# Kernel tuning notes

Measured on AMD Instinct MI355X. Metric: run time of the kernel, lower is better.

The kernel has to match this reference:

```python
import jax, jax.numpy as jnp
import numpy as np

V, E, H, L = 32000, 512, 512, 2   # vocab, emb_dim, hidden_dim, lstm layers
IN = 2 * H                        # input_size (= enc_output feature dim)
B, S_ENC, T_DEC = 32, 128, 64


def setup_inputs() -> dict:
    key = jax.random.key(0)
    ks = jax.random.split(key, 20)
    sc = 0.05
    inp = {
        "tokens": jax.random.randint(ks[0], (B, T_DEC), 0, V),
        "enc_output": jax.random.normal(ks[1], (B, S_ENC, IN), jnp.float32),
        "enc_h": jax.random.normal(ks[2], (L, B, H), jnp.float32),
        "enc_c": jax.random.normal(ks[3], (L, B, H), jnp.float32),
        "emb": jax.random.normal(ks[4], (V, E), jnp.float32) * sc,
        # attention MLP: attn1 in = H*L + IN, out = 4H; attn2: 4H -> 1
        "attn1_w": jax.random.normal(ks[5], (4 * H, H * L + IN), jnp.float32) * sc,
        "attn1_b": jnp.zeros((4 * H,), jnp.float32),
        "attn2_w": jax.random.normal(ks[6], (1, 4 * H), jnp.float32) * sc,
        "attn2_b": jnp.zeros((1,), jnp.float32),
        # LSTM layer 0: input E + IN; layer 1: input H. PyTorch gate order i,f,g,o
        "w_ih0": jax.random.normal(ks[7], (4 * H, E + IN), jnp.float32) * sc,
        "w_hh0": jax.random.normal(ks[8], (4 * H, H), jnp.float32) * sc,
        "b_ih0": jnp.zeros((4 * H,), jnp.float32),
        "b_hh0": jnp.zeros((4 * H,), jnp.float32),
        "w_ih1": jax.random.normal(ks[9], (4 * H, H), jnp.float32) * sc,
        "w_hh1": jax.random.normal(ks[10], (4 * H, H), jnp.float32) * sc,
        "b_ih1": jnp.zeros((4 * H,), jnp.float32),
        "b_hh1": jnp.zeros((4 * H,), jnp.float32),
        "out_w": jax.random.normal(ks[11], (V, H), jnp.float32) * sc,
        "out_b": jnp.zeros((V,), jnp.float32),
    }
    return inp


def _lstm_cell(x, h, c, w_ih, w_hh, b_ih, b_hh):
    g = x @ w_ih.T + h @ w_hh.T + (b_ih + b_hh)
    i, f, gg, o = jnp.split(g, 4, axis=-1)
    c_new = jax.nn.sigmoid(f) * c + jax.nn.sigmoid(i) * jnp.tanh(gg)
    h_new = jax.nn.sigmoid(o) * jnp.tanh(c_new)
    return h_new, c_new


def reference(tokens, enc_output, enc_h, enc_c, emb,
              attn1_w, attn1_b, attn2_w, attn2_b,
              w_ih0, w_hh0, b_ih0, b_hh0,
              w_ih1, w_hh1, b_ih1, b_hh1,
              out_w, out_b):
    b, s_enc = enc_output.shape[0], enc_output.shape[1]

    def context(h):  # h: [L, B, H] -> context: [B, 2H]
        hflat = jnp.transpose(h, (1, 0, 2)).reshape(b, -1)          # [B, L*H]
        hexp = jnp.broadcast_to(hflat[:, None, :], (b, s_enc, hflat.shape[-1]))
        ai = jnp.concatenate([enc_output, hexp], axis=-1)           # [B, S, 2H+L*H]
        hid = ai @ attn1_w.T + attn1_b                               # [B, S, 4H]
        logits = hid @ attn2_w.T + attn2_b                           # [B, S, 1]
        w = jax.nn.softmax(logits, axis=1)
        return jnp.sum(enc_output * w, axis=1)                       # [B, 2H]

    def step(carry, emb_t):  # emb_t: [B, E]
        h, c = carry
        ctx = context(h)
        x = jnp.concatenate([emb_t, ctx], axis=-1)                   # [B, E+2H]
        h0, c0 = _lstm_cell(x, h[0], c[0], w_ih0, w_hh0, b_ih0, b_hh0)
        h1, c1 = _lstm_cell(h0, h[1], c[1], w_ih1, w_hh1, b_ih1, b_hh1)
        return (jnp.stack([h0, h1]), jnp.stack([c0, c1])), h1

    emb_seq = jnp.transpose(emb[tokens], (1, 0, 2))                  # [T, B, E]
    _, outs = jax.lax.scan(step, (enc_h, enc_c), emb_seq)            # [T, B, H]
    dec = jnp.transpose(outs, (1, 0, 2))                             # [B, T, H]
    return dec @ out_w.T + out_b                                     # [B, T, V]
```

## Files before the change

kernel.cpp:

```cpp
#include <hip/hip_runtime.h>
#include <hip/hip_bf16.h>

typedef __attribute__((ext_vector_type(4))) float f4v;
typedef __attribute__((ext_vector_type(4))) short s4v;
typedef __attribute__((ext_vector_type(8))) short s8v;

#define DEVINL __device__ __forceinline__
#define NBLK 128
#define PADK 536
#define WROWS (16 * PADK)
#define HSLOT 16384

DEVINL short f2bf(float f) {
  unsigned u = __float_as_uint(f);
  u += 0x7FFFu + ((u >> 16) & 1u);
  return (short)(u >> 16);
}
DEVINL float bf2f(short s) {
  return __uint_as_float(((unsigned)(unsigned short)s) << 16);
}
DEVINL float sigm(float x) { return 1.f / (1.f + expf(-x)); }

DEVINL void cstore64(short* p, unsigned long long d) {
  asm volatile("global_store_dwordx2 %0, %1, off sc0 sc1"
               :: "v"(p), "v"(d) : "memory");
}

__global__ __launch_bounds__(256) void k_init2(const float* __restrict__ enc_h,
                                               short* __restrict__ hbuf,
                                               unsigned* __restrict__ arr) {
  int i = blockIdx.x * 256 + threadIdx.x;
  hbuf[i] = f2bf(enc_h[i]);
  hbuf[(long)65 * HSLOT + i] = f2bf(enc_h[16384 + i]);
  if (i < NBLK * 32 + 32) arr[i] = 0u;
}

__global__ __launch_bounds__(256) void k_weff(const float* __restrict__ attn1_w,
                                              const float* __restrict__ attn2_w,
                                              float* __restrict__ w_enc) {
  __shared__ float part[8][32];
  int t = threadIdx.x;
  int jl = t & 31, kp = t >> 5;
  int j = blockIdx.x * 32 + jl;
  float acc = 0.f;
  for (int k = kp * 256; k < kp * 256 + 256; ++k)
    acc += attn2_w[k] * attn1_w[(long)k * 2048 + j];
  part[kp][jl] = acc;
  __syncthreads();
  if (t < 32) {
    float s = 0.f;
    for (int p = 0; p < 8; ++p) s += part[p][t];
    w_enc[blockIdx.x * 32 + t] = s;
  }
}

__global__ __launch_bounds__(256) void k_attn_lg(const float* __restrict__ enc,
                                                 const float* __restrict__ w_enc,
                                                 float* __restrict__ logits) {
  __shared__ float red[16][17];
  int b = blockIdx.x >> 3, sp = blockIdx.x & 7;
  int t = threadIdx.x, row = t >> 4, kc = t & 15;
  int s = sp * 16 + row;
  const float* e = enc + ((long)b * 128 + s) * 1024 + kc * 64;
  const float* wv = w_enc + kc * 64;
  float acc = 0.f;
  for (int k = 0; k < 64; k += 4) {
    f4v ev = *(const f4v*)(e + k);
    f4v w4 = *(const f4v*)(wv + k);
    acc += ev[0] * w4[0] + ev[1] * w4[1] + ev[2] * w4[2] + ev[3] * w4[3];
  }
  red[row][kc] = acc;
  __syncthreads();
  if (kc == 0) {
    float sm = 0.f;
#pragma unroll
    for (int i = 0; i < 16; ++i) sm += red[row][i];
    logits[b * 128 + s] = sm;
  }
}

__global__ __launch_bounds__(256) void k_attn_cx(const float* __restrict__ enc,
                                                 const float* __restrict__ logits,
                                                 float* __restrict__ ctx) {
  __shared__ float wls[128];
  __shared__ float red[256];
  int b = blockIdx.x >> 2, ch = blockIdx.x & 3;
  int t = threadIdx.x;
  float lv = (t < 128) ? logits[b * 128 + t] : -3.4e38f;
  red[t] = lv;
  __syncthreads();
  for (int off = 128; off >= 1; off >>= 1) {
    if (t < off) red[t] = fmaxf(red[t], red[t + off]);
    __syncthreads();
  }
  float mx = red[0];
  __syncthreads();
  float ex = 0.f;
  if (t < 128) { ex = expf(lv - mx); wls[t] = ex; }
  red[t] = ex;
  __syncthreads();
  for (int off = 128; off >= 1; off >>= 1) {
    if (t < off) red[t] += red[t + off];
    __syncthreads();
  }
  float inv = 1.f / red[0];
  int dim = ch * 256 + t;
  const float* eb = enc + (long)b * 131072 + dim;
  float a = 0.f;
#pragma unroll 4
  for (int ss = 0; ss < 128; ++ss) a += wls[ss] * eb[ss * 1024];
  ctx[b * 1024 + dim] = a * inv;
}

__global__ __launch_bounds__(256) void k_ctxpre(const float* __restrict__ w_ih0,
                                                const float* __restrict__ b_ih0,
                                                const float* __restrict__ b_hh0,
                                                const float* __restrict__ ctx,
                                                float* __restrict__ ctxpre) {
  int t = threadIdx.x;
  int j = blockIdx.x * 8 + (t >> 5);
  int b = t & 31;
  float acc = b_ih0[j] + b_hh0[j];
  const float* w = w_ih0 + (long)j * 1536 + 512;
  const float* c = ctx + b * 1024;
  for (int k = 0; k < 1024; k += 4) {
    f4v wv = *(const f4v*)(w + k);
    f4v cv = *(const f4v*)(c + k);
    acc += wv[0] * cv[0] + wv[1] * cv[1] + wv[2] * cv[2] + wv[3] * cv[3];
  }
  ctxpre[b * 2048 + j] = acc;
}

__global__ __launch_bounds__(256) void k_cvt(const float* __restrict__ src,
                                             short* __restrict__ dst) {
  long i = ((long)blockIdx.x * 256 + threadIdx.x) * 8;
  f4v a = *(const f4v*)(src + i);
  f4v b = *(const f4v*)(src + i + 4);
  s8v o;
  o[0] = f2bf(a[0]); o[1] = f2bf(a[1]); o[2] = f2bf(a[2]); o[3] = f2bf(a[3]);
  o[4] = f2bf(b[0]); o[5] = f2bf(b[1]); o[6] = f2bf(b[2]); o[7] = f2bf(b[3]);
  *(s8v*)(dst + i) = o;
}

template <int MODE>
__global__ __launch_bounds__(256) void gemm_bf16(
    const float* __restrict__ A, const float* __restrict__ B,
    const int* __restrict__ a_rows, const float* __restrict__ bias,
    float* __restrict__ C, int K, int lda, int ldb, int ldc) {
  __shared__ short As[128 * 72];
  __shared__ short Bs[128 * 72];
  int n0 = blockIdx.x * 128, m0 = blockIdx.y * 128;
  int t = threadIdx.x;
  int lane = t & 63, w = t >> 6;
  int wm = w & 1, wn = w >> 1;
  f4v acc[4][4];
#pragma unroll
  for (int mi = 0; mi < 4; ++mi)
#pragma unroll
    for (int ni = 0; ni < 4; ++ni) acc[mi][ni] = (f4v){0.f, 0.f, 0.f, 0.f};

  int sr = t >> 1;
  int sh = (t & 1) * 32;
  long arow = a_rows ? (long)a_rows[m0 + sr] : (long)(m0 + sr);
  const float* ap = A + arow * lda + sh;
  const float* bp = B + (long)(n0 + sr) * ldb + sh;
  short* as = &As[sr * 72 + sh];
  short* bs = &Bs[sr * 72 + sh];

  for (int k0 = 0; k0 < K; k0 += 64) {
#pragma unroll
    for (int i = 0; i < 8; ++i) {
      f4v va = *(const f4v*)(ap + k0 + i * 4);
      f4v vb = *(const f4v*)(bp + k0 + i * 4);
      s4v sa, sb;
      sa[0] = f2bf(va[0]); sa[1] = f2bf(va[1]); sa[2] = f2bf(va[2]); sa[3] = f2bf(va[3]);
      sb[0] = f2bf(vb[0]); sb[1] = f2bf(vb[1]); sb[2] = f2bf(vb[2]); sb[3] = f2bf(vb[3]);
      *(s4v*)(as + i * 4) = sa;
      *(s4v*)(bs + i * 4) = sb;
    }
    __syncthreads();
#pragma unroll
    for (int ks = 0; ks < 2; ++ks) {
      s8v af[4], bf[4];
#pragma unroll
      for (int mi = 0; mi < 4; ++mi)
        af[mi] = *(const s8v*)&As[(wm * 64 + mi * 16 + (lane & 15)) * 72 + ks * 32 + (lane >> 4) * 8];
#pragma unroll
      for (int ni = 0; ni < 4; ++ni)
        bf[ni] = *(const s8v*)&Bs[(wn * 64 + ni * 16 + (lane & 15)) * 72 + ks * 32 + (lane >> 4) * 8];
#pragma unroll
      for (int mi = 0; mi < 4; ++mi)
#pragma unroll
        for (int ni = 0; ni < 4; ++ni)
          acc[mi][ni] = __builtin_amdgcn_mfma_f32_16x16x32_bf16(af[mi], bf[ni], acc[mi][ni], 0, 0, 0);
    }
    __syncthreads();
  }
  int fq = lane >> 4, fr = lane & 15;
#pragma unroll
  for (int mi = 0; mi < 4; ++mi)
#pragma unroll
    for (int ni = 0; ni < 4; ++ni) {
      int col = n0 + wn * 64 + ni * 16 + fr;
      long rowb = m0 + wm * 64 + mi * 16 + fq * 4;
      if (MODE == 2) {
        int bz = (col & 511) >> 2;
        int c = ((col >> 9) << 2) + (col & 3);
#pragma unroll
        for (int r = 0; r < 4; ++r) {
          long m = rowb + r;
          C[(long)bz * 32768 + (m & 63) * 512 + (m >> 6) * 16 + c] = acc[mi][ni][r];
        }
      } else {
        float bv = bias ? bias[col] : 0.f;
#pragma unroll
        for (int r = 0; r < 4; ++r) C[(rowb + r) * (long)ldc + col] = acc[mi][ni][r] + bv;
      }
    }
}

template <bool BCVT>
__global__ __launch_bounds__(256) void gemm_out(
    const short* __restrict__ A, const short* __restrict__ Bbf,
    const float* __restrict__ Bf, const float* __restrict__ bias,
    float* __restrict__ C) {
  __shared__ short As[128 * 72];
  __shared__ short Bs[128 * 72];
  int m0 = blockIdx.x * 128, n0 = blockIdx.y * 128;
  int t = threadIdx.x;
  int lane = t & 63, w = t >> 6;
  int wm = w & 1, wn = w >> 1;
  f4v acc[4][4];
#pragma unroll
  for (int mi = 0; mi < 4; ++mi)
#pragma unroll
    for (int ni = 0; ni < 4; ++ni) acc[mi][ni] = (f4v){0.f, 0.f, 0.f, 0.f};

  int sr = t >> 1;
  int sh = (t & 1) * 32;
  const short* ap = A + (long)(m0 + sr) * 512 + sh;
  const short* bpb = Bbf + (long)(n0 + sr) * 512 + sh;
  const float* bpf = Bf + (long)(n0 + sr) * 512 + sh;
  short* as = &As[sr * 72 + sh];
  short* bs = &Bs[sr * 72 + sh];

  for (int k0 = 0; k0 < 512; k0 += 64) {
#pragma unroll
    for (int i = 0; i < 4; ++i)
      *(s8v*)(as + i * 8) = *(const s8v*)(ap + k0 + i * 8);
    if (BCVT) {
#pragma unroll
      for (int i = 0; i < 8; ++i) {
        f4v vb = *(const f4v*)(bpf + k0 + i * 4);
        s4v sb;
        sb[0] = f2bf(vb[0]); sb[1] = f2bf(vb[1]); sb[2] = f2bf(vb[2]); sb[3] = f2bf(vb[3]);
        *(s4v*)(bs + i * 4) = sb;
      }
    } else {
#pragma unroll
      for (int i = 0; i < 4; ++i)
        *(s8v*)(bs + i * 8) = *(const s8v*)(bpb + k0 + i * 8);
    }
    __syncthreads();
#pragma unroll
    for (int ks = 0; ks < 2; ++ks) {
      s8v af[4], bf[4];
#pragma unroll
      for (int mi = 0; mi < 4; ++mi)
        af[mi] = *(const s8v*)&As[(wm * 64 + mi * 16 + (lane & 15)) * 72 + ks * 32 + (lane >> 4) * 8];
#pragma unroll
      for (int ni = 0; ni < 4; ++ni)
        bf[ni] = *(const s8v*)&Bs[(wn * 64 + ni * 16 + (lane & 15)) * 72 + ks * 32 + (lane >> 4) * 8];
#pragma unroll
      for (int mi = 0; mi < 4; ++mi)
#pragma unroll
        for (int ni = 0; ni < 4; ++ni)
          acc[mi][ni] = __builtin_amdgcn_mfma_f32_16x16x32_bf16(af[mi], bf[ni], acc[mi][ni], 0, 0, 0);
    }
    __syncthreads();
  }
  int fq = lane >> 4, fr = lane & 15;
#pragma unroll
  for (int mi = 0; mi < 4; ++mi)
#pragma unroll
    for (int ni = 0; ni < 4; ++ni) {
      int col = n0 + wn * 64 + ni * 16 + fr;
      float bv = bias[col];
      long rowb = m0 + wm * 64 + mi * 16 + fq * 4;
#pragma unroll
      for (int r = 0; r < 4; ++r)
        __builtin_nontemporal_store(acc[mi][ni][r] + bv, &C[(rowb + r) * 32000L + col]);
    }
}

__global__ __launch_bounds__(256, 1) void lstm_persist(
    const float* __restrict__ w_hh0, const float* __restrict__ w_ih1,
    const float* __restrict__ w_hh1,
    const float* __restrict__ b_ih1, const float* __restrict__ b_hh1,
    const float* __restrict__ enc_c,
    const float* __restrict__ embp2, const float* __restrict__ ctxpre,
    short* __restrict__ hbuf, short* __restrict__ h1seqbf,
    unsigned* __restrict__ arr) {
  __shared__ alignas(16) short wlds[6 * WROWS];
  __shared__ float ctxp_l[32][16];
  __shared__ float bias1_l[16];
  __shared__ float gbuf[2][32][17];

  const int tid = threadIdx.x;
  const bool is_l0 = (blockIdx.x < NBLK);
  const int bz = is_l0 ? blockIdx.x : blockIdx.x - NBLK;
  const int hb4 = bz * 4;
  const int lane = tid & 63, wid = tid >> 6;
  const int mt = wid & 1, kh = wid >> 1;
  const int fr = lane & 15, fq = lane >> 4;

  const int nmat = is_l0 ? 1 : 2;
  for (int base = tid * 4; base < nmat * 16 * 512; base += 1024) {
    int row = base >> 9, k = base & 511;
    int m = row >> 4, c = row & 15;
    int j = ((c >> 2) << 9) + hb4 + (c & 3);
    const float* wsrc = is_l0 ? w_hh0 : (m == 0 ? w_ih1 : w_hh1);
    f4v v = *(const f4v*)(wsrc + (long)j * 512 + k);
    short* hi = &wlds[(m * 2) * WROWS + c * PADK + k];
    short* lo = &wlds[(m * 2 + 1) * WROWS + c * PADK + k];
#pragma unroll
    for (int e = 0; e < 4; ++e) {
      short hh = f2bf(v[e]);
      hi[e] = hh;
      lo[e] = f2bf(v[e] - bf2f(hh));
    }
  }
  if (is_l0) {
    for (int i = tid; i < 512; i += 256) {
      int b = i >> 4, c = i & 15;
      ctxp_l[b][c] = ctxpre[b * 2048 + ((c >> 2) << 9) + hb4 + (c & 3)];
    }
  } else if (tid < 16) {
    int j = ((tid >> 2) << 9) + hb4 + (tid & 3);
    bias1_l[tid] = b_ih1[j] + b_hh1[j];
  }
  const int cq = (tid & 127) >> 2, cr = tid & 3;
  float cst = 0.f;
  if (tid < 128)
    cst = enc_c[(is_l0 ? 0 : 16384) + cq * 512 + hb4 + cr];
  __syncthreads();
  asm volatile("s_waitcnt vmcnt(0)" ::: "memory");
  asm volatile("buffer_inv sc1" ::: "memory");
  __syncthreads();

  short* H0 = hbuf;
  short* H1 = hbuf + (long)65 * HSLOT;
  const int foff = (mt * 16 + fr) * 512 + kh * 256 + fq * 8;
  const int woff = fr * PADK + kh * 256 + fq * 8;

  if (is_l0) {
    for (int p = 0; p < 64; ++p) {
      float e4[4];
      if (tid < 128) {
        const float* ep = embp2 + (long)bz * 32768 + p * 512 + cq * 16 + cr;
#pragma unroll
        for (int g = 0; g < 4; ++g) e4[g] = ep[g * 4];
      }
      if (p) {
        if (tid < NBLK)
          while (__hip_atomic_load(&arr[tid << 5], __ATOMIC_RELAXED,
                                   __HIP_MEMORY_SCOPE_AGENT) < (unsigned)p)
            __builtin_amdgcn_s_sleep(1);
        __syncthreads();
      }
      const short* a0 = H0 + (long)p * HSLOT + foff;
      f4v l0h = {0.f, 0.f, 0.f, 0.f}, l0l = l0h;
      const short* b0h = &wlds[0 * WROWS + woff];
      const short* b0l = &wlds[1 * WROWS + woff];
#pragma unroll
      for (int ks = 0; ks < 8; ++ks) {
        s8v A0 = *(const s8v*)(a0 + ks * 32);
        s8v B0h = *(const s8v*)(b0h + ks * 32);
        s8v B0l = *(const s8v*)(b0l + ks * 32);
        l0h = __builtin_amdgcn_mfma_f32_16x16x32_bf16(A0, B0h, l0h, 0, 0, 0);
        l0l = __builtin_amdgcn_mfma_f32_16x16x32_bf16(A0, B0l, l0l, 0, 0, 0);
      }
      f4v s = l0h + l0l;
#pragma unroll
      for (int r = 0; r < 4; ++r) gbuf[kh][mt * 16 + fq * 4 + r][fr] = s[r];
      __syncthreads();
      if (tid < 128) {
        float g4[4];
#pragma unroll
        for (int g = 0; g < 4; ++g) {
          int c = g * 4 + cr;
          g4[g] = gbuf[0][cq][c] + gbuf[1][cq][c] + ctxp_l[cq][c] + e4[g];
        }
        float cn = sigm(g4[1]) * cst + sigm(g4[0]) * tanhf(g4[2]);
        float hn = sigm(g4[3]) * tanhf(cn);
        cst = cn;
        unsigned v16 = (unsigned)(unsigned short)f2bf(hn);
        unsigned p01 = v16 | ((unsigned)__shfl_down((int)v16, 1) << 16);
        unsigned long long wd = (unsigned long long)p01 |
            ((unsigned long long)(unsigned)__shfl_down((int)p01, 2) << 32);
        if ((tid & 3) == 0)
          cstore64(H0 + (long)(p + 1) * HSLOT + cq * 512 + hb4, wd);
      }
      asm volatile("s_waitcnt vmcnt(0)" ::: "memory");
      __syncthreads();
      if (tid == 0)
        __hip_atomic_store(&arr[(unsigned)bz << 5], (unsigned)(p + 1),
                           __ATOMIC_RELAXED, __HIP_MEMORY_SCOPE_AGENT);
    }
  } else {
    for (int p = 1; p <= 64; ++p) {
      if (tid < NBLK)
        while (__hip_atomic_load(&arr[tid << 5], __ATOMIC_RELAXED,
                                 __HIP_MEMORY_SCOPE_AGENT) < (unsigned)p)
          __builtin_amdgcn_s_sleep(2);
      __syncthreads();
      const short* a0 = H0 + (long)p * HSLOT + foff;
      f4v x1h = {0.f, 0.f, 0.f, 0.f}, x1l = x1h, h1h = x1h, h1l = x1h;
      const short* b2h = &wlds[0 * WROWS + woff];
      const short* b2l = &wlds[1 * WROWS + woff];
#pragma unroll
      for (int ks = 0; ks < 8; ++ks) {
        s8v A0 = *(const s8v*)(a0 + ks * 32);
        s8v B2h = *(const s8v*)(b2h + ks * 32);
        s8v B2l = *(const s8v*)(b2l + ks * 32);
        x1h = __builtin_amdgcn_mfma_f32_16x16x32_bf16(A0, B2h, x1h, 0, 0, 0);
        x1l = __builtin_amdgcn_mfma_f32_16x16x32_bf16(A0, B2l, x1l, 0, 0, 0);
      }
      if (p > 1) {
        if (tid < NBLK)
          while (__hip_atomic_load(&arr[(tid << 5) + 16], __ATOMIC_RELAXED,
                                   __HIP_MEMORY_SCOPE_AGENT) < (unsigned)(p - 1))
            __builtin_amdgcn_s_sleep(2);
        __syncthreads();
      }
      const short* a1 = H1 + (long)(p - 1) * HSLOT + foff;
      const short* b4h = &wlds[2 * WROWS + woff];
      const short* b4l = &wlds[3 * WROWS + woff];
#pragma unroll
      for (int ks = 0; ks < 8; ++ks) {
        s8v A1 = *(const s8v*)(a1 + ks * 32);
        s8v B4h = *(const s8v*)(b4h + ks * 32);
        s8v B4l = *(const s8v*)(b4l + ks * 32);
        h1h = __builtin_amdgcn_mfma_f32_16x16x32_bf16(A1, B4h, h1h, 0, 0, 0);
        h1l = __builtin_amdgcn_mfma_f32_16x16x32_bf16(A1, B4l, h1l, 0, 0, 0);
      }
      f4v s = x1h + x1l + h1h + h1l;
#pragma unroll
      for (int r = 0; r < 4; ++r) gbuf[kh][mt * 16 + fq * 4 + r][fr] = s[r];
      __syncthreads();
      if (tid < 128) {
        float g4[4];
#pragma unroll
        for (int g = 0; g < 4; ++g) {
          int c = g * 4 + cr;
          g4[g] = gbuf[0][cq][c] + gbuf[1][cq][c] + bias1_l[c];
        }
        float cn = sigm(g4[1]) * cst + sigm(g4[0]) * tanhf(g4[2]);
        float hn = sigm(g4[3]) * tanhf(cn);
        cst = cn;
        unsigned v16 = (unsigned)(unsigned short)f2bf(hn);
        unsigned p01 = v16 | ((unsigned)__shfl_down((int)v16, 1) << 16);
        unsigned long long wd = (unsigned long long)p01 |
            ((unsigned long long)(unsigned)__shfl_down((int)p01, 2) << 32);
        if ((tid & 3) == 0) {
          if (p < 64)
            cstore64(H1 + (long)p * HSLOT + cq * 512 + hb4, wd);
          *(unsigned long long*)&h1seqbf[((long)cq * 64 + (p - 1)) * 512 + hb4] = wd;
        }
      }
      if (p < 64) {
        asm volatile("s_waitcnt vmcnt(0)" ::: "memory");
        __syncthreads();
        if (tid == 0)
          __hip_atomic_store(&arr[((unsigned)bz << 5) + 16], (unsigned)p,
                             __ATOMIC_RELAXED, __HIP_MEMORY_SCOPE_AGENT);
      }
    }
  }
}

extern "C" void kernel_launch(void* const* d_in, const int* in_sizes, int n_in,
                              void* d_out, int out_size, void* d_ws, size_t ws_size,
                              hipStream_t stream) {
  const int*   tokens  = (const int*)  d_in[0];
  const float* enc_out = (const float*)d_in[1];
  const float* enc_h   = (const float*)d_in[2];
  const float* enc_c   = (const float*)d_in[3];
  const float* emb     = (const float*)d_in[4];
  const float* attn1_w = (const float*)d_in[5];
  const float* attn2_w = (const float*)d_in[7];
  const float* w_ih0   = (const float*)d_in[9];
  const float* w_hh0   = (const float*)d_in[10];
  const float* b_ih0   = (const float*)d_in[11];
  const float* b_hh0   = (const float*)d_in[12];
  const float* w_ih1   = (const float*)d_in[13];
  const float* w_hh1   = (const float*)d_in[14];
  const float* b_ih1   = (const float*)d_in[15];
  const float* b_hh1   = (const float*)d_in[16];
  const float* out_w   = (const float*)d_in[17];
  const float* out_b   = (const float*)d_in[18];
  float* out = (float*)d_out;

  float* f = (float*)d_ws;
  float*    w_enc    = f;
  float*    ctx      = f + 1024;
  float*    ctxpre   = f + 33792;
  float*    embp2    = f + 99328;
  short*    h1seqbf  = (short*)(f + 4293632);
  short*    hbuf     = (short*)(f + 4817920);
  unsigned* arr      = (unsigned*)(f + 5882880);
  float*    logits   = f + 5887040;
  short*    out_w_bf = (short*)(f + 5891200);
  const size_t NEED = (size_t)(5891200 + 8192000) * 4;
  const bool big = ws_size >= NEED;

  k_init2<<<64, 256, 0, stream>>>(enc_h, hbuf, arr);
  k_weff<<<32, 256, 0, stream>>>(attn1_w, attn2_w, w_enc);
  k_attn_lg<<<256, 256, 0, stream>>>(enc_out, w_enc, logits);
  k_attn_cx<<<128, 256, 0, stream>>>(enc_out, logits, ctx);
  k_ctxpre<<<256, 256, 0, stream>>>(w_ih0, b_ih0, b_hh0, ctx, ctxpre);
  gemm_bf16<2><<<dim3(16, 16), 256, 0, stream>>>(emb, w_ih0, tokens, nullptr,
                                                 embp2, 512, 512, 1536, 0);
  if (big) k_cvt<<<8000, 256, 0, stream>>>(out_w, out_w_bf);
  lstm_persist<<<2 * NBLK, 256, 0, stream>>>(w_hh0, w_ih1, w_hh1, b_ih1, b_hh1,
                                             enc_c, embp2, ctxpre, hbuf,
                                             h1seqbf, arr);
  if (big)
    gemm_out<false><<<dim3(16, 250), 256, 0, stream>>>(h1seqbf, out_w_bf, nullptr,
                                                       out_b, out);
  else
    gemm_out<true><<<dim3(16, 250), 256, 0, stream>>>(h1seqbf, nullptr, out_w,
                                                      out_b, out);
}
```

Baseline: 547.2 us.

## Restructure persistent LSTM kernel to 128 threads with weight-as-A MFMA and no LDS reduction

The persistent LSTM recurrence kernel drops from 256 to 128 threads per block. Each wave now covers a 16-batch slice over the full K=512 range instead of splitting K across waves, with the weights as the MFMA A operand and h as B. Permuting the weight rows puts each lane's four gates directly in its accumulator registers. This removes the gbuf LDS cross-wave reduction and one __syncthreads per step, shortening the serial per-step critical path. In exchange each wave runs twice as many dependent MFMAs per step, holds 16 s8v h fragments in registers, and all 128 threads now spin on the arrival flags.

New measurement: 628.9 us. 1.15x slower.

```diff
diff --git a/kernel.cpp b/kernel.cpp
--- a/kernel.cpp
+++ b/kernel.cpp
@@ -293,7 +293,7 @@
     }
 }
 
-__global__ __launch_bounds__(256, 1) void lstm_persist(
+__global__ __launch_bounds__(128, 1) void lstm_persist(
     const float* __restrict__ w_hh0, const float* __restrict__ w_ih1,
     const float* __restrict__ w_hh1,
     const float* __restrict__ b_ih1, const float* __restrict__ b_hh1,
@@ -301,24 +301,23 @@
     const float* __restrict__ embp2, const float* __restrict__ ctxpre,
     short* __restrict__ hbuf, short* __restrict__ h1seqbf,
     unsigned* __restrict__ arr) {
-  __shared__ alignas(16) short wlds[6 * WROWS];
-  __shared__ float ctxp_l[32][16];
+  __shared__ alignas(16) short wlds[4 * WROWS];
+  __shared__ float ctxp_l[32][17];
   __shared__ float bias1_l[16];
-  __shared__ float gbuf[2][32][17];
 
   const int tid = threadIdx.x;
   const bool is_l0 = (blockIdx.x < NBLK);
   const int bz = is_l0 ? blockIdx.x : blockIdx.x - NBLK;
   const int hb4 = bz * 4;
-  const int lane = tid & 63, wid = tid >> 6;
-  const int mt = wid & 1, kh = wid >> 1;
+  const int lane = tid & 63, w = tid >> 6;
   const int fr = lane & 15, fq = lane >> 4;
+  const int batch = w * 16 + fr;
 
   const int nmat = is_l0 ? 1 : 2;
-  for (int base = tid * 4; base < nmat * 16 * 512; base += 1024) {
+  for (int base = tid * 4; base < nmat * 16 * 512; base += 512) {
     int row = base >> 9, k = base & 511;
     int m = row >> 4, c = row & 15;
-    int j = ((c >> 2) << 9) + hb4 + (c & 3);
+    int j = ((c & 3) << 9) + hb4 + (c >> 2);
     const float* wsrc = is_l0 ? w_hh0 : (m == 0 ? w_ih1 : w_hh1);
     f4v v = *(const f4v*)(wsrc + (long)j * 512 + k);
     short* hi = &wlds[(m * 2) * WROWS + c * PADK + k];
@@ -331,7 +330,7 @@
     }
   }
   if (is_l0) {
-    for (int i = tid; i < 512; i += 256) {
+    for (int i = tid; i < 512; i += 128) {
       int b = i >> 4, c = i & 15;
       ctxp_l[b][c] = ctxpre[b * 2048 + ((c >> 2) << 9) + hb4 + (c & 3)];
     }
@@ -339,10 +338,7 @@
     int j = ((tid >> 2) << 9) + hb4 + (tid & 3);
     bias1_l[tid] = b_ih1[j] + b_hh1[j];
   }
-  const int cq = (tid & 127) >> 2, cr = tid & 3;
-  float cst = 0.f;
-  if (tid < 128)
-    cst = enc_c[(is_l0 ? 0 : 16384) + cq * 512 + hb4 + cr];
+  float cst = enc_c[(is_l0 ? 0 : 16384) + batch * 512 + hb4 + fq];
   __syncthreads();
   asm volatile("s_waitcnt vmcnt(0)" ::: "memory");
   asm volatile("buffer_inv sc1" ::: "memory");
@@ -350,57 +346,51 @@
 
   short* H0 = hbuf;
   short* H1 = hbuf + (long)65 * HSLOT;
-  const int foff = (mt * 16 + fr) * 512 + kh * 256 + fq * 8;
-  const int woff = fr * PADK + kh * 256 + fq * 8;
+  const int boff = batch * 512 + fq * 8;
+  const int woff = fr * PADK + fq * 8;
 
   if (is_l0) {
     for (int p = 0; p < 64; ++p) {
       float e4[4];
-      if (tid < 128) {
-        const float* ep = embp2 + (long)bz * 32768 + p * 512 + cq * 16 + cr;
+      {
+        const float* ep = embp2 + (long)bz * 32768 + p * 512 + batch * 16 + fq;
 #pragma unroll
         for (int g = 0; g < 4; ++g) e4[g] = ep[g * 4];
       }
       if (p) {
-        if (tid < NBLK)
-          while (__hip_atomic_load(&arr[tid << 5], __ATOMIC_RELAXED,
-                                   __HIP_MEMORY_SCOPE_AGENT) < (unsigned)p)
-            __builtin_amdgcn_s_sleep(1);
+        while (__hip_atomic_load(&arr[tid << 5], __ATOMIC_RELAXED,
+                                 __HIP_MEMORY_SCOPE_AGENT) < (unsigned)p)
+          __builtin_amdgcn_s_sleep(1);
         __syncthreads();
       }
-      const short* a0 = H0 + (long)p * HSLOT + foff;
-      f4v l0h = {0.f, 0.f, 0.f, 0.f}, l0l = l0h;
+      const short* a0 = H0 + (long)p * HSLOT + boff;
+      s8v B0[16];
+#pragma unroll
+      for (int ks = 0; ks < 16; ++ks) B0[ks] = *(const s8v*)(a0 + ks * 32);
+      f4v ah = {0.f, 0.f, 0.f, 0.f}, al = ah;
       const short* b0h = &wlds[0 * WROWS + woff];
       const short* b0l = &wlds[1 * WROWS + woff];
 #pragma unroll
-      for (int ks = 0; ks < 8; ++ks) {
-        s8v A0 = *(const s8v*)(a0 + ks * 32);
-        s8v B0h = *(const s8v*)(b0h + ks * 32);
-        s8v B0l = *(const s8v*)(b0l + ks * 32);
-        l0h = __builtin_amdgcn_mfma_f32_16x16x32_bf16(A0, B0h, l0h, 0, 0, 0);
-        l0l = __builtin_amdgcn_mfma_f32_16x16x32_bf16(A0, B0l, l0l, 0, 0, 0);
-      }
-      f4v s = l0h + l0l;
-#pragma unroll
-      for (int r = 0; r < 4; ++r) gbuf[kh][mt * 16 + fq * 4 + r][fr] = s[r];
-      __syncthreads();
-      if (tid < 128) {
-        float g4[4];
-#pragma unroll
-        for (int g = 0; g < 4; ++g) {
-          int c = g * 4 + cr;
-          g4[g] = gbuf[0][cq][c] + gbuf[1][cq][c] + ctxp_l[cq][c] + e4[g];
-        }
-        float cn = sigm(g4[1]) * cst + sigm(g4[0]) * tanhf(g4[2]);
-        float hn = sigm(g4[3]) * tanhf(cn);
-        cst = cn;
-        unsigned v16 = (unsigned)(unsigned short)f2bf(hn);
-        unsigned p01 = v16 | ((unsigned)__shfl_down((int)v16, 1) << 16);
-        unsigned long long wd = (unsigned long long)p01 |
-            ((unsigned long long)(unsigned)__shfl_down((int)p01, 2) << 32);
-        if ((tid & 3) == 0)
-          cstore64(H0 + (long)(p + 1) * HSLOT + cq * 512 + hb4, wd);
-      }
+      for (int ks = 0; ks < 16; ++ks) {
+        s8v Wh = *(const s8v*)(b0h + ks * 32);
+        s8v Wl = *(const s8v*)(b0l + ks * 32);
+        ah = __builtin_amdgcn_mfma_f32_16x16x32_bf16(Wh, B0[ks], ah, 0, 0, 0);
+        al = __builtin_amdgcn_mfma_f32_16x16x32_bf16(Wl, B0[ks], al, 0, 0, 0);
+      }
+      f4v gs = ah + al;
+      float g4[4];
+#pragma unroll
+      for (int g = 0; g < 4; ++g)
+        g4[g] = gs[g] + ctxp_l[batch][g * 4 + fq] + e4[g];
+      float cn = sigm(g4[1]) * cst + sigm(g4[0]) * tanhf(g4[2]);
+      float hn = sigm(g4[3]) * tanhf(cn);
+      cst = cn;
+      unsigned v16 = (unsigned)(unsigned short)f2bf(hn);
+      unsigned p01 = v16 | ((unsigned)__shfl_down((int)v16, 16) << 16);
+      unsigned long long wd = (unsigned long long)p01 |
+          ((unsigned long long)(unsigned)__shfl_down((int)p01, 32) << 32);
+      if (lane < 16)
+        cstore64(H0 + (long)(p + 1) * HSLOT + batch * 512 + hb4, wd);
       asm volatile("s_waitcnt vmcnt(0)" ::: "memory");
       __syncthreads();
       if (tid == 0)
@@ -409,64 +399,57 @@
     }
   } else {
     for (int p = 1; p <= 64; ++p) {
-      if (tid < NBLK)
-        while (__hip_atomic_load(&arr[tid << 5], __ATOMIC_RELAXED,
-                                 __HIP_MEMORY_SCOPE_AGENT) < (unsigned)p)
-          __builtin_amdgcn_s_sleep(2);
+      while (__hip_atomic_load(&arr[tid << 5], __ATOMIC_RELAXED,
+                               __HIP_MEMORY_SCOPE_AGENT) < (unsigned)p)
+        __builtin_amdgcn_s_sleep(2);
       __syncthreads();
-      const short* a0 = H0 + (long)p * HSLOT + foff;
-      f4v x1h = {0.f, 0.f, 0.f, 0.f}, x1l = x1h, h1h = x1h, h1l = x1h;
+      const short* a0 = H0 + (long)p * HSLOT + boff;
+      s8v BF[16];
+#pragma unroll
+      for (int ks = 0; ks < 16; ++ks) BF[ks] = *(const s8v*)(a0 + ks * 32);
+      f4v ah = {0.f, 0.f, 0.f, 0.f}, al = ah;
       const short* b2h = &wlds[0 * WROWS + woff];
       const short* b2l = &wlds[1 * WROWS + woff];
 #pragma unroll
-      for (int ks = 0; ks < 8; ++ks) {
-        s8v A0 = *(const s8v*)(a0 + ks * 32);
-        s8v B2h = *(const s8v*)(b2h + ks * 32);
-        s8v B2l = *(const s8v*)(b2l + ks * 32);
-        x1h = __builtin_amdgcn_mfma_f32_16x16x32_bf16(A0, B2h, x1h, 0, 0, 0);
-        x1l = __builtin_amdgcn_mfma_f32_16x16x32_bf16(A0, B2l, x1l, 0, 0, 0);
+      for (int ks = 0; ks < 16; ++ks) {
+        s8v Wh = *(const s8v*)(b2h + ks * 32);
+        s8v Wl = *(const s8v*)(b2l + ks * 32);
+        ah = __builtin_amdgcn_mfma_f32_16x16x32_bf16(Wh, BF[ks], ah, 0, 0, 0);
+        al = __builtin_amdgcn_mfma_f32_16x16x32_bf16(Wl, BF[ks], al, 0, 0, 0);
       }
       if (p > 1) {
-        if (tid < NBLK)
-          while (__hip_atomic_load(&arr[(tid << 5) + 16], __ATOMIC_RELAXED,
-                                   __HIP_MEMORY_SCOPE_AGENT) < (unsigned)(p - 1))
-            __builtin_amdgcn_s_sleep(2);
+        while (__hip_atomic_load(&arr[(tid << 5) + 16], __ATOMIC_RELAXED,
+                                 __HIP_MEMORY_SCOPE_AGENT) < (unsigned)(p - 1))
+          __builtin_amdgcn_s_sleep(2);
         __syncthreads();
       }
-      const short* a1 = H1 + (long)(p - 1) * HSLOT + foff;
+      const short* a1 = H1 + (long)(p - 1) * HSLOT + boff;
+#pragma unroll
+      for (int ks = 0; ks < 16; ++ks) BF[ks] = *(const s8v*)(a1 + ks * 32);
       const short* b4h = &wlds[2 * WROWS + woff];
       const short* b4l = &wlds[3 * WROWS + woff];
 #pragma unroll
-      for (int ks = 0; ks < 8; ++ks) {
-        s8v A1 = *(const s8v*)(a1 + ks * 32);
-        s8v B4h = *(const s8v*)(b4h + ks * 32);
-        s8v B4l = *(const s8v*)(b4l + ks * 32);
-        h1h = __builtin_amdgcn_mfma_f32_16x16x32_bf16(A1, B4h, h1h, 0, 0, 0);
-        h1l = __builtin_amdgcn_mfma_f32_16x16x32_bf16(A1, B4l, h1l, 0, 0, 0);
-      }
-      f4v s = x1h + x1l + h1h + h1l;
-#pragma unroll
-      for (int r = 0; r < 4; ++r) gbuf[kh][mt * 16 + fq * 4 + r][fr] = s[r];
-      __syncthreads();
-      if (tid < 128) {
-        float g4[4];
-#pragma unroll
-        for (int g = 0; g < 4; ++g) {
-          int c = g * 4 + cr;
-          g4[g] = gbuf[0][cq][c] + gbuf[1][cq][c] + bias1_l[c];
-        }
-        float cn = sigm(g4[1]) * cst + sigm(g4[0]) * tanhf(g4[2]);
-        float hn = sigm(g4[3]) * tanhf(cn);
-        cst = cn;
-        unsigned v16 = (unsigned)(unsigned short)f2bf(hn);
-        unsigned p01 = v16 | ((unsigned)__shfl_down((int)v16, 1) << 16);
-        unsigned long long wd = (unsigned long long)p01 |
-            ((unsigned long long)(unsigned)__shfl_down((int)p01, 2) << 32);
-        if ((tid & 3) == 0) {
-          if (p < 64)
-            cstore64(H1 + (long)p * HSLOT + cq * 512 + hb4, wd);
-          *(unsigned long long*)&h1seqbf[((long)cq * 64 + (p - 1)) * 512 + hb4] = wd;
-        }
+      for (int ks = 0; ks < 16; ++ks) {
+        s8v Wh = *(const s8v*)(b4h + ks * 32);
+        s8v Wl = *(const s8v*)(b4l + ks * 32);
+        ah = __builtin_amdgcn_mfma_f32_16x16x32_bf16(Wh, BF[ks], ah, 0, 0, 0);
+        al = __builtin_amdgcn_mfma_f32_16x16x32_bf16(Wl, BF[ks], al, 0, 0, 0);
+      }
+      f4v gs = ah + al;
+      float g4[4];
+#pragma unroll
+      for (int g = 0; g < 4; ++g) g4[g] = gs[g] + bias1_l[g * 4 + fq];
+      float cn = sigm(g4[1]) * cst + sigm(g4[0]) * tanhf(g4[2]);
+      float hn = sigm(g4[3]) * tanhf(cn);
+      cst = cn;
+      unsigned v16 = (unsigned)(unsigned short)f2bf(hn);
+      unsigned p01 = v16 | ((unsigned)__shfl_down((int)v16, 16) << 16);
+      unsigned long long wd = (unsigned long long)p01 |
+          ((unsigned long long)(unsigned)__shfl_down((int)p01, 32) << 32);
+      if (lane < 16) {
+        if (p < 64)
+          cstore64(H1 + (long)p * HSLOT + batch * 512 + hb4, wd);
+        *(unsigned long long*)&h1seqbf[((long)batch * 64 + (p - 1)) * 512 + hb4] = wd;
       }
       if (p < 64) {
         asm volatile("s_waitcnt vmcnt(0)" ::: "memory");
@@ -522,7 +505,7 @@
   gemm_bf16<2><<<dim3(16, 16), 256, 0, stream>>>(emb, w_ih0, tokens, nullptr,
                                                  embp2, 512, 512, 1536, 0);
   if (big) k_cvt<<<8000, 256, 0, stream>>>(out_w, out_w_bf);
-  lstm_persist<<<2 * NBLK, 256, 0, stream>>>(w_hh0, w_ih1, w_hh1, b_ih1, b_hh1,
+  lstm_persist<<<2 * NBLK, 128, 0, stream>>>(w_hh0, w_ih1, w_hh1, b_ih1, b_hh1,
                                              enc_c, embp2, ctxpre, hbuf,
                                              h1seqbf, arr);
   if (big)
```
